# Optimization experiments

Measured on AMD Instinct MI355X. Metric: run time of the kernel, lower is better.

Reference implementation:

```python
import jax, jax.numpy as jnp
import numpy as np


def conv_t(x, w, stride, padding):
    """torch.nn.functional.conv_transpose2d equivalent.
    w is in torch ConvTranspose2d layout [C_in, C_out, kh, kw]."""
    k = w.shape[2]
    kern = jnp.flip(w, (2, 3)).transpose(1, 0, 2, 3)  # -> OIHW
    pad = k - 1 - padding
    return jax.lax.conv_general_dilated(
        x, kern,
        window_strides=(1, 1),
        padding=[(pad, pad), (pad, pad)],
        lhs_dilation=(stride, stride),
        dimension_numbers=('NCHW', 'OIHW', 'NCHW'))


def setup_inputs() -> dict:
    key = jax.random.key(0)
    ks = jax.random.split(key, 4)
    B, planes, inplanes, H = 32, 256, 128, 28
    x = jax.random.normal(ks[0], (B, planes, H, H), dtype=jnp.float32)
    # torch ConvTranspose2d weight layout: [in, out, kh, kw]
    w_conv2 = jax.random.normal(ks[1], (planes, planes, 3, 3), dtype=jnp.float32) * 0.02
    w_conv1 = jax.random.normal(ks[2], (planes, inplanes, 3, 3), dtype=jnp.float32) * 0.02
    w_up = jax.random.normal(ks[3], (planes // 2, inplanes, 2, 2), dtype=jnp.float32) * 0.02
    # Fixup init: biases zero, scale one
    z = jnp.zeros((1,), dtype=jnp.float32)
    return {
        'x': x, 'w_conv2': w_conv2, 'w_conv1': w_conv1, 'w_up': w_up,
        'bias1a': z, 'bias1b': z, 'bias2a': z, 'bias2b': z,
        'scale': jnp.ones((1,), dtype=jnp.float32),
    }


def reference(x, w_conv2, w_conv1, w_up, bias1a, bias1b, bias2a, bias2b, scale):
    # main branch
    out = conv_t(x + bias1a, w_conv2, stride=1, padding=1)        # [B,planes,H,W]
    out = jax.nn.relu(out + bias1b)
    out = conv_t(out + bias2a, w_conv1, stride=2, padding=1)      # [B,inplanes,2H-1,2W-1]
    out = out * scale + bias2b

    # upsample branch: keep the C/2 channels with the largest (max - min) range,
    # per sample, in ascending-range order (matches np.argsort(diff)[C/2:]).
    C = x.shape[1]
    rng = jnp.max(x, axis=(2, 3)) - jnp.min(x, axis=(2, 3))       # [B,C]
    idx = jnp.argsort(rng, axis=1)[:, C // 2:]                    # [B,C/2]
    x_sel = jnp.take_along_axis(x, idx[:, :, None, None], axis=1)  # [B,C/2,H,W]
    identity = conv_t(x_sel + bias1a, w_up, stride=2, padding=0)  # [B,inplanes,2H,2W]

    # pad main branch top-left by 1 to match 2H x 2W
    out = jnp.pad(out, ((0, 0), (0, 0), (1, 0), (1, 0)))
    out = jax.nn.relu(out + identity)
    return out
```

## Files before the change

### kernel.cpp

```cpp
#include <hip/hip_runtime.h>

#define NB 32
#define NC 256
#define NO 128
#define HH 28
#define HW 784
#define OH 56

typedef unsigned short u16;
typedef __attribute__((ext_vector_type(8))) short bf16x8;
typedef __attribute__((ext_vector_type(4))) float f32x4;
typedef __attribute__((ext_vector_type(8))) unsigned short u16x8;

#define MFMA(A,B,C) __builtin_amdgcn_mfma_f32_16x16x32_bf16(A,B,C,0,0,0)

__device__ __forceinline__ u16 f2bf(float f) {
    unsigned u = __float_as_uint(f);
    unsigned r = (u + 0x7fffu + ((u >> 16) & 1u)) >> 16;
    return (u16)r;
}

__global__ void k_misc(const float* __restrict__ w2, const float* __restrict__ w1,
                       const float* __restrict__ wup,
                       u16* __restrict__ wT2, u16* __restrict__ wc2T,
                       u16* __restrict__ wupT, uint4* __restrict__ r1T4) {
    int blk = blockIdx.x;
    if (blk < 288) {
        int g = blk * 256 + threadIdx.x;
        int o = g & 255;
        int cb = (g >> 8) & 31;
        int tap = g >> 13;
        int u = 2 - tap / 3, v = 2 - tap % 3;
        u16x8 out;
#pragma unroll
        for (int ci = 0; ci < 8; ++ci) {
            int c = cb * 8 + ci;
            out[ci] = f2bf(w2[((c * NC + o) * 3 + u) * 3 + v]);
        }
        *(u16x8*)(wT2 + (size_t)g * 8) = out;
    } else if (blk < 432) {
        const int taps[9] = {0, 2, 6, 8, 1, 7, 3, 5, 4};
        int g = (blk - 288) * 256 + threadIdx.x;
        int o = g & 127;
        int cb = (g >> 7) & 31;
        int s = g >> 12;
        int tap = taps[s];
        u16x8 out;
#pragma unroll
        for (int ci = 0; ci < 8; ++ci) {
            int c = cb * 8 + ci;
            out[ci] = f2bf(w1[(c * NO + o) * 9 + tap]);
        }
        *(u16x8*)(wc2T + (size_t)g * 8) = out;
    } else if (blk < 464) {
        int g = (blk - 432) * 256 + threadIdx.x;
        int o = g & 127;
        int kb = (g >> 7) & 15;
        int p = g >> 11;
        u16x8 out;
#pragma unroll
        for (int ki = 0; ki < 8; ++ki) {
            int k = kb * 8 + ki;
            out[ki] = f2bf(wup[(k * NO + o) * 4 + p]);
        }
        *(u16x8*)(wupT + (size_t)g * 8) = out;
    } else {
        int g = (blk - 464) * 256 + threadIdx.x;
        int i = g % 176;
        int bc = g / 176;
        int b = bc >> 5, cb = bc & 31;
        int row, cx;
        if (i < 32)      { row = 0;  cx = i; }
        else if (i < 64) { row = 29; cx = i - 32; }
        else {
            int j = i - 64;
            row = 1 + (j >> 2);
            int k = j & 3;
            cx = (k == 0) ? 0 : 28 + k;
        }
        r1T4[((b * 30 + row) * 32 + cb) * 32 + cx] = make_uint4(0, 0, 0, 0);
    }
}

__global__ __launch_bounds__(256) void k_prep_x(
    const float* __restrict__ x, const float* __restrict__ pb1a,
    u16* __restrict__ xT2, float* __restrict__ rng)
{
    __shared__ float sx[8][HW];
    __shared__ float smx[8][4], smn[8][4];
    int t = threadIdx.x;
    int b = blockIdx.x >> 5, cb = blockIdx.x & 31;
    float b1a = pb1a[0];
    const float* xb = x + ((size_t)b * NC + cb * 8) * HW;

    float mx[8], mn[8];
#pragma unroll
    for (int ci = 0; ci < 8; ++ci) { mx[ci] = -1e30f; mn[ci] = 1e30f; }
#pragma unroll
    for (int ci = 0; ci < 8; ++ci) {
        for (int px = t; px < HW; px += 256) {
            float v = xb[ci * HW + px];
            sx[ci][px] = v;
            mx[ci] = fmaxf(mx[ci], v);
            mn[ci] = fminf(mn[ci], v);
        }
    }
    int lane = t & 63, wv = t >> 6;
#pragma unroll
    for (int ci = 0; ci < 8; ++ci) {
        float a = mx[ci], i = mn[ci];
        for (int off = 32; off; off >>= 1) {
            a = fmaxf(a, __shfl_down(a, off, 64));
            i = fminf(i, __shfl_down(i, off, 64));
        }
        if (lane == 0) { smx[ci][wv] = a; smn[ci][wv] = i; }
    }
    __syncthreads();
    if (t < 8) {
        float a = fmaxf(fmaxf(smx[t][0], smx[t][1]), fmaxf(smx[t][2], smx[t][3]));
        float i = fminf(fminf(smn[t][0], smn[t][1]), fminf(smn[t][2], smn[t][3]));
        rng[b * NC + cb * 8 + t] = a - i;
    }
    for (int g = t; g < 960; g += 256) {
        int ry = g >> 5, cx = g & 31;
        int y = ry - 1, xx = cx - 1;
        bool valid = (y >= 0 && y < HH && xx >= 0 && xx < HH);
        u16x8 out;
#pragma unroll
        for (int ci = 0; ci < 8; ++ci) {
            float f = valid ? sx[ci][y * 28 + xx] + b1a : 0.f;
            out[ci] = f2bf(f);
        }
        *(u16x8*)(xT2 + ((((size_t)b * 30 + ry) * 32 + cb) * 32 + cx) * 8) = out;
    }
}

__global__ void k_pack_xup(const float* __restrict__ x, const int* __restrict__ sel,
                           const float* __restrict__ pb1a, u16* __restrict__ xupT) {
    int g = blockIdx.x * 256 + threadIdx.x;
    float b1a = pb1a[0];
    int cx = g & 31;
    int kb = (g >> 5) & 15;
    int qyb = g >> 9;
    int b = qyb / 28;
    int qy = qyb - b * 28;
    bool valid = cx < 28;
    const int* selb = sel + b * NO;
    const float* xb = x + (size_t)b * NC * HW + qy * 28 + (valid ? cx : 0);
    u16x8 out;
#pragma unroll
    for (int ki = 0; ki < 8; ++ki) {
        int ch = selb[kb * 8 + ki];
        float f = valid ? xb[ch * HW] + b1a : 0.f;
        out[ki] = f2bf(f);
    }
    *(u16x8*)(xupT + (size_t)g * 8) = out;
}

__global__ void k_select(const float* __restrict__ rng, int* __restrict__ sel) {
    int b = blockIdx.x;
    int c = threadIdx.x;
    __shared__ float s[NC];
    s[c] = rng[b * NC + c];
    __syncthreads();
    float v = s[c];
    int rank = 0;
    for (int j = 0; j < NC; ++j) {
        float u = s[j];
        rank += (u < v) || (u == v && j < c);
    }
    if (rank >= NC / 2) sel[b * (NC / 2) + (rank - NC / 2)] = c;
}

__global__ __launch_bounds__(512, 4) void k_conv1_mfma(
    const u16* __restrict__ xT2, const u16* __restrict__ wT2,
    const float* __restrict__ pb1b, const float* __restrict__ pb2a,
    u16* __restrict__ r1T)
{
    __shared__ u16 sA[6 * 16 * 32 * 8];
    int tid = threadIdx.x;
    int wave = tid >> 6, lane = tid & 63;
    int wpi = wave >> 2;
    int wo = wave & 3;
    int l15 = lane & 15, lg = lane >> 4;

    int idx = blockIdx.x;
    int b = idx / 14;
    int rem = idx - b * 14;
    int rg = rem >> 1;
    int og = rem & 1;
    int y0 = rg * 4;

    float b1b = pb1b[0], b2a = pb2a[0];

    int bOff[2];
#pragma unroll
    for (int ot = 0; ot < 2; ++ot)
        bOff[ot] = (lg * 256 + (og * 128 + wo * 32 + ot * 16 + l15)) * 16;

    f32x4 acc[4][2] = {};
    const char* wq = (const char*)wT2;
    const char* ap0 = (const char*)sA;
    const uint4* gx = (const uint4*)xT2;
    uint4* dst = (uint4*)sA;

    for (int half = 0; half < 2; ++half) {
        if (half) __syncthreads();
#pragma unroll
        for (int i = 0; i < 6; ++i)
            dst[tid + i * 512] = gx[(b * 30 + y0 + i) * 1024 + half * 512 + tid];
        __syncthreads();

        for (int cc = 0; cc < 128; cc += 32) {
            int c0 = half * 128 + cc;
#pragma unroll
            for (int dy = 0; dy < 3; ++dy) {
#pragma unroll
                for (int dx = 0; dx < 3; ++dx) {
                    int tap = dy * 3 + dx;
                    bf16x8 w[2];
#pragma unroll
                    for (int ot = 0; ot < 2; ++ot)
                        w[ot] = *(const bf16x8*)(wq + (bOff[ot] + tap * 131072 + c0 * 512));
                    bf16x8 a[2][2];
#pragma unroll
                    for (int m = 0; m < 2; ++m)
#pragma unroll
                        for (int h = 0; h < 2; ++h)
                            a[m][h] = *(const bf16x8*)(ap0 +
                                (2 * wpi + m + dy) * 8192 + cc * 64 + lg * 512 +
                                (h * 16 + l15 + dx) * 16);
#pragma unroll
                    for (int m = 0; m < 2; ++m)
#pragma unroll
                        for (int h = 0; h < 2; ++h)
#pragma unroll
                            for (int ot = 0; ot < 2; ++ot)
                                acc[m * 2 + h][ot] = MFMA(a[m][h], w[ot], acc[m * 2 + h][ot]);
                }
            }
        }
    }

#pragma unroll
    for (int m = 0; m < 2; ++m)
#pragma unroll
        for (int h = 0; h < 2; ++h) {
            int y = y0 + 2 * wpi + m;
            int x0 = h * 16 + lg * 4;
            if (x0 >= 28) continue;
#pragma unroll
            for (int ot = 0; ot < 2; ++ot) {
                int o = og * 128 + wo * 32 + ot * 16 + l15;
                size_t base = ((((size_t)b * 30 + y + 1) * 32 + (o >> 3)) * 32 + (x0 + 1)) * 8 + (o & 7);
#pragma unroll
                for (int r = 0; r < 4; ++r) {
                    float f = fmaxf(acc[m * 2 + h][ot][r] + b1b, 0.f) + b2a;
                    r1T[base + (size_t)r * 8] = f2bf(f);
                }
            }
        }
}

__global__ __launch_bounds__(512, 2) void k_conv2_mfma(
    const u16* __restrict__ r1T, const u16* __restrict__ xupT,
    const u16* __restrict__ wc2T, const u16* __restrict__ wupT,
    const float* __restrict__ pscale, const float* __restrict__ pb2b,
    float* __restrict__ out)
{
    __shared__ uint4 sA2[5120];
    int tid = threadIdx.x;
    int wave = tid >> 6, lane = tid & 63;
    int wpi = wave >> 2;
    int wo = wave & 3;
    int l15 = lane & 15, lg = lane >> 4;

    int b = blockIdx.x / 7;
    int rg = blockIdx.x - b * 7;
    int y0 = rg * 4;

    float scale = pscale[0], b2b = pb2b[0];

    {
        const uint4* src = (const uint4*)(r1T + (size_t)(b * 30 + y0) * 8192);
#pragma unroll
        for (int i = 0; i < 10; ++i)
            sA2[tid + i * 512] = src[tid + i * 512];
    }
    __syncthreads();

    f32x4 acc[4][4][2] = {};

    const char* sp = (const char*)sA2;
    const char* wp = (const char*)wc2T;

    int aBase[4];
#pragma unroll
    for (int pt = 0; pt < 4; ++pt) {
        int rel = 2 * wpi + (pt >> 1) + 1;
        int qt = pt & 1;
        aBase[pt] = ((rel * 32 + lg) * 32 + (qt * 16 + l15 + 1)) * 16;
    }
    int bBase = (lg * 128 + wo * 32 + l15) * 16;

    for (int c0 = 0; c0 < 256; c0 += 32) {
        bf16x8 w[9][2];
#pragma unroll
        for (int s = 0; s < 9; ++s)
#pragma unroll
            for (int ot = 0; ot < 2; ++ot)
                w[s][ot] = *(const bf16x8*)(wp + (bBase + s * 65536 + c0 * 256 + ot * 256));
#pragma unroll
        for (int pt = 0; pt < 4; ++pt) {
            const char* ap = sp + (aBase[pt] + c0 * 64);
            bf16x8 aD = *(const bf16x8*)(ap);
            bf16x8 aC = *(const bf16x8*)(ap - 16);
            bf16x8 aB = *(const bf16x8*)(ap - 16384);
            bf16x8 aA = *(const bf16x8*)(ap - 16400);
#pragma unroll
            for (int ot = 0; ot < 2; ++ot) {
                acc[0][pt][ot] = MFMA(aD, w[0][ot], acc[0][pt][ot]);
                acc[0][pt][ot] = MFMA(aC, w[1][ot], acc[0][pt][ot]);
                acc[0][pt][ot] = MFMA(aB, w[2][ot], acc[0][pt][ot]);
                acc[0][pt][ot] = MFMA(aA, w[3][ot], acc[0][pt][ot]);
                acc[1][pt][ot] = MFMA(aD, w[4][ot], acc[1][pt][ot]);
                acc[1][pt][ot] = MFMA(aB, w[5][ot], acc[1][pt][ot]);
                acc[2][pt][ot] = MFMA(aD, w[6][ot], acc[2][pt][ot]);
                acc[2][pt][ot] = MFMA(aC, w[7][ot], acc[2][pt][ot]);
                acc[3][pt][ot] = MFMA(aD, w[8][ot], acc[3][pt][ot]);
            }
        }
    }

#pragma unroll
    for (int pt = 0; pt < 4; ++pt) {
        int qy = y0 + 2 * wpi + (pt >> 1);
        int qt = pt & 1;
        int qx0 = qt * 16 + lg * 4;
        bool zr = (qy == 0);
#pragma unroll
        for (int ot = 0; ot < 2; ++ot)
#pragma unroll
            for (int r = 0; r < 4; ++r) {
                bool zc = (qx0 + r == 0);
                float a0 = acc[0][pt][ot][r], a1 = acc[1][pt][ot][r];
                float a2 = acc[2][pt][ot][r], a3 = acc[3][pt][ot][r];
                acc[0][pt][ot][r] = (zr || zc) ? 0.f : fmaf(a0, scale, b2b);
                acc[1][pt][ot][r] = zr ? 0.f : fmaf(a1, scale, b2b);
                acc[2][pt][ot][r] = zc ? 0.f : fmaf(a2, scale, b2b);
                acc[3][pt][ot][r] = fmaf(a3, scale, b2b);
            }
    }

    const char* up = (const char*)xupT;
    const char* wu = (const char*)wupT;
    int uBaseA[4];
#pragma unroll
    for (int pt = 0; pt < 4; ++pt) {
        int qy = y0 + 2 * wpi + (pt >> 1);
        int qt = pt & 1;
        uBaseA[pt] = (((b * 28 + qy) * 16 + lg) * 32 + (qt * 16 + l15)) * 16;
    }
    for (int k0 = 0; k0 < 128; k0 += 32) {
        bf16x8 wb[4][2];
#pragma unroll
        for (int p = 0; p < 4; ++p)
#pragma unroll
            for (int ot = 0; ot < 2; ++ot)
                wb[p][ot] = *(const bf16x8*)(wu + (bBase + p * 32768 + k0 * 256 + ot * 256));
#pragma unroll
        for (int pt = 0; pt < 4; ++pt) {
            bf16x8 aU = *(const bf16x8*)(up + (uBaseA[pt] + k0 * 64));
#pragma unroll
            for (int p = 0; p < 4; ++p)
#pragma unroll
                for (int ot = 0; ot < 2; ++ot)
                    acc[p][pt][ot] = MFMA(aU, wb[p][ot], acc[p][pt][ot]);
        }
    }

#pragma unroll
    for (int pt = 0; pt < 4; ++pt) {
        int qy = y0 + 2 * wpi + (pt >> 1);
        int qt = pt & 1;
        int qx0 = qt * 16 + lg * 4;
        if (qx0 >= 28) continue;
#pragma unroll
        for (int ot = 0; ot < 2; ++ot) {
            int o = wo * 32 + ot * 16 + l15;
            size_t base = ((size_t)(b * NO + o) * OH + 2 * qy) * OH + 2 * qx0;
#pragma unroll
            for (int r = 0; r < 4; ++r) {
                float2 v0 = { fmaxf(acc[0][pt][ot][r], 0.f), fmaxf(acc[1][pt][ot][r], 0.f) };
                float2 v1 = { fmaxf(acc[2][pt][ot][r], 0.f), fmaxf(acc[3][pt][ot][r], 0.f) };
                *reinterpret_cast<float2*>(&out[base + 2 * r]) = v0;
                *reinterpret_cast<float2*>(&out[base + OH + 2 * r]) = v1;
            }
        }
    }
}

extern "C" void kernel_launch(void* const* d_in, const int* in_sizes, int n_in,
                              void* d_out, int out_size, void* d_ws, size_t ws_size,
                              hipStream_t stream)
{
    const float* x     = (const float*)d_in[0];
    const float* w2    = (const float*)d_in[1];
    const float* w1    = (const float*)d_in[2];
    const float* wup   = (const float*)d_in[3];
    const float* b1a   = (const float*)d_in[4];
    const float* b1b   = (const float*)d_in[5];
    const float* b2a   = (const float*)d_in[6];
    const float* b2b   = (const float*)d_in[7];
    const float* scale = (const float*)d_in[8];

    char* ws = (char*)d_ws;
    u16* xT2   = (u16*)(ws);
    u16* r1T   = (u16*)(ws + 15728640);
    u16* xupT  = (u16*)(ws + 31457280);
    u16* wT2   = (u16*)(ws + 38797312);
    u16* wc2T  = (u16*)(ws + 39976960);
    u16* wupT  = (u16*)(ws + 40566784);
    float* rng = (float*)(ws + 40697856);
    int* sel   = (int*)(ws + 40730624);
    float* out = (float*)d_out;

    hipLaunchKernelGGL(k_misc, dim3(1168), dim3(256), 0, stream,
                       w2, w1, wup, wT2, wc2T, wupT, (uint4*)r1T);
    hipLaunchKernelGGL(k_prep_x, dim3(1024), dim3(256), 0, stream, x, b1a, xT2, rng);
    hipLaunchKernelGGL(k_select, dim3(NB), dim3(NC), 0, stream, rng, sel);
    hipLaunchKernelGGL(k_pack_xup, dim3(1792), dim3(256), 0, stream, x, sel, b1a, xupT);
    hipLaunchKernelGGL(k_conv1_mfma, dim3(448), dim3(512), 0, stream,
                       xT2, wT2, b1b, b2a, r1T);
    hipLaunchKernelGGL(k_conv2_mfma, dim3(NB * 7), dim3(512), 0, stream,
                       r1T, xupT, wc2T, wupT, scale, b2b, out);
}
```

Before: 114.3 us.

## Fuse xup packing into conv1 launch and split conv2 across output-channel halves

```diff
diff --git a/kernel.cpp b/kernel.cpp
--- a/kernel.cpp
+++ b/kernel.cpp
@@ -135,28 +135,6 @@
     }
 }
 
-__global__ void k_pack_xup(const float* __restrict__ x, const int* __restrict__ sel,
-                           const float* __restrict__ pb1a, u16* __restrict__ xupT) {
-    int g = blockIdx.x * 256 + threadIdx.x;
-    float b1a = pb1a[0];
-    int cx = g & 31;
-    int kb = (g >> 5) & 15;
-    int qyb = g >> 9;
-    int b = qyb / 28;
-    int qy = qyb - b * 28;
-    bool valid = cx < 28;
-    const int* selb = sel + b * NO;
-    const float* xb = x + (size_t)b * NC * HW + qy * 28 + (valid ? cx : 0);
-    u16x8 out;
-#pragma unroll
-    for (int ki = 0; ki < 8; ++ki) {
-        int ch = selb[kb * 8 + ki];
-        float f = valid ? xb[ch * HW] + b1a : 0.f;
-        out[ki] = f2bf(f);
-    }
-    *(u16x8*)(xupT + (size_t)g * 8) = out;
-}
-
 __global__ void k_select(const float* __restrict__ rng, int* __restrict__ sel) {
     int b = blockIdx.x;
     int c = threadIdx.x;
@@ -172,12 +150,36 @@
     if (rank >= NC / 2) sel[b * (NC / 2) + (rank - NC / 2)] = c;
 }
 
-__global__ __launch_bounds__(512, 4) void k_conv1_mfma(
+__global__ __launch_bounds__(512, 4) void k_conv1x(
     const u16* __restrict__ xT2, const u16* __restrict__ wT2,
     const float* __restrict__ pb1b, const float* __restrict__ pb2a,
-    u16* __restrict__ r1T)
+    u16* __restrict__ r1T,
+    const float* __restrict__ x, const int* __restrict__ sel,
+    const float* __restrict__ pb1a, u16* __restrict__ xupT)
 {
     __shared__ u16 sA[6 * 16 * 32 * 8];
+    if (blockIdx.x >= 448) {
+        int g = (blockIdx.x - 448) * 512 + threadIdx.x;
+        float b1a = pb1a[0];
+        int cx = g & 31;
+        int kb = (g >> 5) & 15;
+        int qyb = g >> 9;
+        int b = qyb / 28;
+        int qy = qyb - b * 28;
+        bool valid = cx < 28;
+        const int* selb = sel + b * NO;
+        const float* xb = x + (size_t)b * NC * HW + qy * 28 + (valid ? cx : 0);
+        u16x8 out;
+#pragma unroll
+        for (int ki = 0; ki < 8; ++ki) {
+            int ch = selb[kb * 8 + ki];
+            float f = valid ? xb[ch * HW] + b1a : 0.f;
+            out[ki] = f2bf(f);
+        }
+        *(u16x8*)(xupT + (size_t)g * 8) = out;
+        return;
+    }
+
     int tid = threadIdx.x;
     int wave = tid >> 6, lane = tid & 63;
     int wpi = wave >> 2;
@@ -262,7 +264,7 @@
         }
 }
 
-__global__ __launch_bounds__(512, 2) void k_conv2_mfma(
+__global__ __launch_bounds__(512, 4) void k_conv2_mfma(
     const u16* __restrict__ r1T, const u16* __restrict__ xupT,
     const u16* __restrict__ wc2T, const u16* __restrict__ wupT,
     const float* __restrict__ pscale, const float* __restrict__ pb2b,
@@ -275,8 +277,11 @@
     int wo = wave & 3;
     int l15 = lane & 15, lg = lane >> 4;
 
-    int b = blockIdx.x / 7;
-    int rg = blockIdx.x - b * 7;
+    int idx = blockIdx.x;
+    int b = idx / 14;
+    int rem = idx - b * 14;
+    int rg = rem >> 1;
+    int og = rem & 1;
     int y0 = rg * 4;
 
     float scale = pscale[0], b2b = pb2b[0];
@@ -289,7 +294,7 @@
     }
     __syncthreads();
 
-    f32x4 acc[4][4][2] = {};
+    f32x4 acc[4][4] = {};
 
     const char* sp = (const char*)sA2;
     const char* wp = (const char*)wc2T;
@@ -301,15 +306,13 @@
         int qt = pt & 1;
         aBase[pt] = ((rel * 32 + lg) * 32 + (qt * 16 + l15 + 1)) * 16;
     }
-    int bBase = (lg * 128 + wo * 32 + l15) * 16;
+    int bBase = (lg * 128 + og * 64 + wo * 16 + l15) * 16;
 
     for (int c0 = 0; c0 < 256; c0 += 32) {
-        bf16x8 w[9][2];
+        bf16x8 w[9];
 #pragma unroll
         for (int s = 0; s < 9; ++s)
-#pragma unroll
-            for (int ot = 0; ot < 2; ++ot)
-                w[s][ot] = *(const bf16x8*)(wp + (bBase + s * 65536 + c0 * 256 + ot * 256));
+            w[s] = *(const bf16x8*)(wp + (bBase + s * 65536 + c0 * 256));
 #pragma unroll
         for (int pt = 0; pt < 4; ++pt) {
             const char* ap = sp + (aBase[pt] + c0 * 64);
@@ -317,18 +320,15 @@
             bf16x8 aC = *(const bf16x8*)(ap - 16);
             bf16x8 aB = *(const bf16x8*)(ap - 16384);
             bf16x8 aA = *(const bf16x8*)(ap - 16400);
-#pragma unroll
-            for (int ot = 0; ot < 2; ++ot) {
-                acc[0][pt][ot] = MFMA(aD, w[0][ot], acc[0][pt][ot]);
-                acc[0][pt][ot] = MFMA(aC, w[1][ot], acc[0][pt][ot]);
-                acc[0][pt][ot] = MFMA(aB, w[2][ot], acc[0][pt][ot]);
-                acc[0][pt][ot] = MFMA(aA, w[3][ot], acc[0][pt][ot]);
-                acc[1][pt][ot] = MFMA(aD, w[4][ot], acc[1][pt][ot]);
-                acc[1][pt][ot] = MFMA(aB, w[5][ot], acc[1][pt][ot]);
-                acc[2][pt][ot] = MFMA(aD, w[6][ot], acc[2][pt][ot]);
-                acc[2][pt][ot] = MFMA(aC, w[7][ot], acc[2][pt][ot]);
-                acc[3][pt][ot] = MFMA(aD, w[8][ot], acc[3][pt][ot]);
-            }
+            acc[0][pt] = MFMA(aD, w[0], acc[0][pt]);
+            acc[0][pt] = MFMA(aC, w[1], acc[0][pt]);
+            acc[0][pt] = MFMA(aB, w[2], acc[0][pt]);
+            acc[0][pt] = MFMA(aA, w[3], acc[0][pt]);
+            acc[1][pt] = MFMA(aD, w[4], acc[1][pt]);
+            acc[1][pt] = MFMA(aB, w[5], acc[1][pt]);
+            acc[2][pt] = MFMA(aD, w[6], acc[2][pt]);
+            acc[2][pt] = MFMA(aC, w[7], acc[2][pt]);
+            acc[3][pt] = MFMA(aD, w[8], acc[3][pt]);
         }
     }
 
@@ -339,17 +339,15 @@
         int qx0 = qt * 16 + lg * 4;
         bool zr = (qy == 0);
 #pragma unroll
-        for (int ot = 0; ot < 2; ++ot)
-#pragma unroll
-            for (int r = 0; r < 4; ++r) {
-                bool zc = (qx0 + r == 0);
-                float a0 = acc[0][pt][ot][r], a1 = acc[1][pt][ot][r];
-                float a2 = acc[2][pt][ot][r], a3 = acc[3][pt][ot][r];
-                acc[0][pt][ot][r] = (zr || zc) ? 0.f : fmaf(a0, scale, b2b);
-                acc[1][pt][ot][r] = zr ? 0.f : fmaf(a1, scale, b2b);
-                acc[2][pt][ot][r] = zc ? 0.f : fmaf(a2, scale, b2b);
-                acc[3][pt][ot][r] = fmaf(a3, scale, b2b);
-            }
+        for (int r = 0; r < 4; ++r) {
+            bool zc = (qx0 + r == 0);
+            float a0 = acc[0][pt][r], a1 = acc[1][pt][r];
+            float a2 = acc[2][pt][r], a3 = acc[3][pt][r];
+            acc[0][pt][r] = (zr || zc) ? 0.f : fmaf(a0, scale, b2b);
+            acc[1][pt][r] = zr ? 0.f : fmaf(a1, scale, b2b);
+            acc[2][pt][r] = zc ? 0.f : fmaf(a2, scale, b2b);
+            acc[3][pt][r] = fmaf(a3, scale, b2b);
+        }
     }
 
     const char* up = (const char*)xupT;
@@ -362,20 +360,16 @@
         uBaseA[pt] = (((b * 28 + qy) * 16 + lg) * 32 + (qt * 16 + l15)) * 16;
     }
     for (int k0 = 0; k0 < 128; k0 += 32) {
-        bf16x8 wb[4][2];
+        bf16x8 wb[4];
 #pragma unroll
         for (int p = 0; p < 4; ++p)
-#pragma unroll
-            for (int ot = 0; ot < 2; ++ot)
-                wb[p][ot] = *(const bf16x8*)(wu + (bBase + p * 32768 + k0 * 256 + ot * 256));
+            wb[p] = *(const bf16x8*)(wu + (bBase + p * 32768 + k0 * 256));
 #pragma unroll
         for (int pt = 0; pt < 4; ++pt) {
             bf16x8 aU = *(const bf16x8*)(up + (uBaseA[pt] + k0 * 64));
 #pragma unroll
             for (int p = 0; p < 4; ++p)
-#pragma unroll
-                for (int ot = 0; ot < 2; ++ot)
-                    acc[p][pt][ot] = MFMA(aU, wb[p][ot], acc[p][pt][ot]);
+                acc[p][pt] = MFMA(aU, wb[p], acc[p][pt]);
         }
     }
 
@@ -385,17 +379,14 @@
         int qt = pt & 1;
         int qx0 = qt * 16 + lg * 4;
         if (qx0 >= 28) continue;
-#pragma unroll
-        for (int ot = 0; ot < 2; ++ot) {
-            int o = wo * 32 + ot * 16 + l15;
-            size_t base = ((size_t)(b * NO + o) * OH + 2 * qy) * OH + 2 * qx0;
-#pragma unroll
-            for (int r = 0; r < 4; ++r) {
-                float2 v0 = { fmaxf(acc[0][pt][ot][r], 0.f), fmaxf(acc[1][pt][ot][r], 0.f) };
-                float2 v1 = { fmaxf(acc[2][pt][ot][r], 0.f), fmaxf(acc[3][pt][ot][r], 0.f) };
-                *reinterpret_cast<float2*>(&out[base + 2 * r]) = v0;
-                *reinterpret_cast<float2*>(&out[base + OH + 2 * r]) = v1;
-            }
+        int o = og * 64 + wo * 16 + l15;
+        size_t base = ((size_t)(b * NO + o) * OH + 2 * qy) * OH + 2 * qx0;
+#pragma unroll
+        for (int r = 0; r < 4; ++r) {
+            float2 v0 = { fmaxf(acc[0][pt][r], 0.f), fmaxf(acc[1][pt][r], 0.f) };
+            float2 v1 = { fmaxf(acc[2][pt][r], 0.f), fmaxf(acc[3][pt][r], 0.f) };
+            *reinterpret_cast<float2*>(&out[base + 2 * r]) = v0;
+            *reinterpret_cast<float2*>(&out[base + OH + 2 * r]) = v1;
         }
     }
 }
@@ -429,9 +420,8 @@
                        w2, w1, wup, wT2, wc2T, wupT, (uint4*)r1T);
     hipLaunchKernelGGL(k_prep_x, dim3(1024), dim3(256), 0, stream, x, b1a, xT2, rng);
     hipLaunchKernelGGL(k_select, dim3(NB), dim3(NC), 0, stream, rng, sel);
-    hipLaunchKernelGGL(k_pack_xup, dim3(1792), dim3(256), 0, stream, x, sel, b1a, xupT);
-    hipLaunchKernelGGL(k_conv1_mfma, dim3(448), dim3(512), 0, stream,
-                       xT2, wT2, b1b, b2a, r1T);
-    hipLaunchKernelGGL(k_conv2_mfma, dim3(NB * 7), dim3(512), 0, stream,
+    hipLaunchKernelGGL(k_conv1x, dim3(1344), dim3(512), 0, stream,
+                       xT2, wT2, b1b, b2a, r1T, x, sel, b1a, xupT);
+    hipLaunchKernelGGL(k_conv2_mfma, dim3(448), dim3(512), 0, stream,
                        r1T, xupT, wc2T, wupT, scale, b2b, out);
 }
```

New measurement: 114.4 us. About the same (+0.1%).

## Fuse xup packing into conv1 and give each block two batches

Applied to the files above, without the earlier changes.

```diff
diff --git a/kernel.cpp b/kernel.cpp
--- a/kernel.cpp
+++ b/kernel.cpp
@@ -135,28 +135,6 @@
     }
 }
 
-__global__ void k_pack_xup(const float* __restrict__ x, const int* __restrict__ sel,
-                           const float* __restrict__ pb1a, u16* __restrict__ xupT) {
-    int g = blockIdx.x * 256 + threadIdx.x;
-    float b1a = pb1a[0];
-    int cx = g & 31;
-    int kb = (g >> 5) & 15;
-    int qyb = g >> 9;
-    int b = qyb / 28;
-    int qy = qyb - b * 28;
-    bool valid = cx < 28;
-    const int* selb = sel + b * NO;
-    const float* xb = x + (size_t)b * NC * HW + qy * 28 + (valid ? cx : 0);
-    u16x8 out;
-#pragma unroll
-    for (int ki = 0; ki < 8; ++ki) {
-        int ch = selb[kb * 8 + ki];
-        float f = valid ? xb[ch * HW] + b1a : 0.f;
-        out[ki] = f2bf(f);
-    }
-    *(u16x8*)(xupT + (size_t)g * 8) = out;
-}
-
 __global__ void k_select(const float* __restrict__ rng, int* __restrict__ sel) {
     int b = blockIdx.x;
     int c = threadIdx.x;
@@ -172,24 +150,49 @@
     if (rank >= NC / 2) sel[b * (NC / 2) + (rank - NC / 2)] = c;
 }
 
-__global__ __launch_bounds__(512, 4) void k_conv1_mfma(
+__global__ __launch_bounds__(512, 4) void k_conv1x(
     const u16* __restrict__ xT2, const u16* __restrict__ wT2,
     const float* __restrict__ pb1b, const float* __restrict__ pb2a,
-    u16* __restrict__ r1T)
+    u16* __restrict__ r1T,
+    const float* __restrict__ x, const int* __restrict__ sel,
+    const float* __restrict__ pb1a, u16* __restrict__ xupT)
 {
-    __shared__ u16 sA[6 * 16 * 32 * 8];
+    __shared__ uint4 sA4[3072];
+    if (blockIdx.x >= 224) {
+        int g = (blockIdx.x - 224) * 512 + threadIdx.x;
+        float b1a = pb1a[0];
+        int cx = g & 31;
+        int kb = (g >> 5) & 15;
+        int qyb = g >> 9;
+        int b = qyb / 28;
+        int qy = qyb - b * 28;
+        bool valid = cx < 28;
+        const int* selb = sel + b * NO;
+        const float* xb = x + (size_t)b * NC * HW + qy * 28 + (valid ? cx : 0);
+        u16x8 out;
+#pragma unroll
+        for (int ki = 0; ki < 8; ++ki) {
+            int ch = selb[kb * 8 + ki];
+            float f = valid ? xb[ch * HW] + b1a : 0.f;
+            out[ki] = f2bf(f);
+        }
+        *(u16x8*)(xupT + (size_t)g * 8) = out;
+        return;
+    }
+
     int tid = threadIdx.x;
     int wave = tid >> 6, lane = tid & 63;
-    int wpi = wave >> 2;
+    int bh = wave >> 2;
     int wo = wave & 3;
     int l15 = lane & 15, lg = lane >> 4;
 
     int idx = blockIdx.x;
-    int b = idx / 14;
-    int rem = idx - b * 14;
+    int bp = idx / 14;
+    int rem = idx - bp * 14;
     int rg = rem >> 1;
     int og = rem & 1;
     int y0 = rg * 4;
+    int b = bp * 2 + bh;
 
     float b1b = pb1b[0], b2a = pb2a[0];
 
@@ -198,21 +201,26 @@
     for (int ot = 0; ot < 2; ++ot)
         bOff[ot] = (lg * 256 + (og * 128 + wo * 32 + ot * 16 + l15)) * 16;
 
-    f32x4 acc[4][2] = {};
+    f32x4 acc[8][2] = {};
     const char* wq = (const char*)wT2;
-    const char* ap0 = (const char*)sA;
+    const char* ap0 = (const char*)sA4 + bh * 24576;
     const uint4* gx = (const uint4*)xT2;
-    uint4* dst = (uint4*)sA;
-
-    for (int half = 0; half < 2; ++half) {
-        if (half) __syncthreads();
-#pragma unroll
-        for (int i = 0; i < 6; ++i)
-            dst[tid + i * 512] = gx[(b * 30 + y0 + i) * 1024 + half * 512 + tid];
+
+    for (int q = 0; q < 4; ++q) {
+        if (q) __syncthreads();
+#pragma unroll
+        for (int i = 0; i < 6; ++i) {
+            int ch = (tid >> 8) + i * 2;
+            int within = tid & 255;
+            int bb = ch / 6, row = ch - (ch / 6) * 6;
+            sA4[ch * 256 + within] =
+                gx[((size_t)(bp * 2 + bb) * 30 + y0 + row) * 1024 + q * 256 + within];
+        }
         __syncthreads();
 
-        for (int cc = 0; cc < 128; cc += 32) {
-            int c0 = half * 128 + cc;
+#pragma unroll
+        for (int cs = 0; cs < 2; ++cs) {
+            int c0 = q * 64 + cs * 32;
 #pragma unroll
             for (int dy = 0; dy < 3; ++dy) {
 #pragma unroll
@@ -222,16 +230,16 @@
 #pragma unroll
                     for (int ot = 0; ot < 2; ++ot)
                         w[ot] = *(const bf16x8*)(wq + (bOff[ot] + tap * 131072 + c0 * 512));
-                    bf16x8 a[2][2];
-#pragma unroll
-                    for (int m = 0; m < 2; ++m)
+                    bf16x8 a[4][2];
+#pragma unroll
+                    for (int m = 0; m < 4; ++m)
 #pragma unroll
                         for (int h = 0; h < 2; ++h)
                             a[m][h] = *(const bf16x8*)(ap0 +
-                                (2 * wpi + m + dy) * 8192 + cc * 64 + lg * 512 +
+                                (m + dy) * 4096 + cs * 2048 + lg * 512 +
                                 (h * 16 + l15 + dx) * 16);
 #pragma unroll
-                    for (int m = 0; m < 2; ++m)
+                    for (int m = 0; m < 4; ++m)
 #pragma unroll
                         for (int h = 0; h < 2; ++h)
 #pragma unroll
@@ -243,10 +251,10 @@
     }
 
 #pragma unroll
-    for (int m = 0; m < 2; ++m)
+    for (int m = 0; m < 4; ++m)
 #pragma unroll
         for (int h = 0; h < 2; ++h) {
-            int y = y0 + 2 * wpi + m;
+            int y = y0 + m;
             int x0 = h * 16 + lg * 4;
             if (x0 >= 28) continue;
 #pragma unroll
@@ -429,9 +437,8 @@
                        w2, w1, wup, wT2, wc2T, wupT, (uint4*)r1T);
     hipLaunchKernelGGL(k_prep_x, dim3(1024), dim3(256), 0, stream, x, b1a, xT2, rng);
     hipLaunchKernelGGL(k_select, dim3(NB), dim3(NC), 0, stream, rng, sel);
-    hipLaunchKernelGGL(k_pack_xup, dim3(1792), dim3(256), 0, stream, x, sel, b1a, xupT);
-    hipLaunchKernelGGL(k_conv1_mfma, dim3(448), dim3(512), 0, stream,
-                       xT2, wT2, b1b, b2a, r1T);
+    hipLaunchKernelGGL(k_conv1x, dim3(1120), dim3(512), 0, stream,
+                       xT2, wT2, b1b, b2a, r1T, x, sel, b1a, xupT);
     hipLaunchKernelGGL(k_conv2_mfma, dim3(NB * 7), dim3(512), 0, stream,
                        r1T, xupT, wc2T, wupT, scale, b2b, out);
 }
```

Result: slower. 171.7 us (+50.1%).
